# Kernel optimization log

Hardware: AMD Instinct MI355X
Metric: run time of the kernel (lower is better)

The kernel has to match this reference:

```python
import jax, jax.numpy as jnp
import numpy as np

HID = 512

def setup_inputs() -> dict:
    key = jax.random.key(0)
    k1, k2, k3, k4, k5, k6 = jax.random.split(key, 6)
    B, T, H = 32, 4096, HID
    enc_seq = jax.random.normal(k1, (B, T, H), dtype=jnp.float32)
    enc_mask = jax.random.randint(k2, (B, T), 0, 2, dtype=jnp.int32)
    dec_state = jax.random.normal(k3, (B, H), dtype=jnp.float32)
    # Linear weights, torch layout: y = x @ W.T
    scale = 1.0 / np.sqrt(H)
    W_h = jax.random.uniform(k4, (H, H), jnp.float32, -scale, scale)
    W_s = jax.random.uniform(k5, (H, H), jnp.float32, -scale, scale)
    v = jax.random.uniform(k6, (H,), jnp.float32, -scale, scale)
    return {"enc_seq": enc_seq, "enc_mask": enc_mask, "dec_state": dec_state,
            "W_h": W_h, "W_s": W_s, "v": v}

def reference(enc_seq, enc_mask, dec_state, W_h, W_s, v):
    # s: [B,H] -> [B,1,H] broadcast over T; h: [B,T,H]
    s = jnp.einsum('bh,kh->bk', dec_state, W_s)[:, None, :]
    h = jnp.einsum('bth,kh->btk', enc_seq, W_h)
    e = jnp.einsum('bth,h->bt', jnp.tanh(h + s), v)  # [B,T]
    e = jnp.where(enc_mask == 0, jnp.float32(-1e9), e)
    a = jax.nn.softmax(e, axis=1)  # [B,T]
    ctx = jnp.einsum('bt,bth->bh', a, enc_seq)  # [B,H]
    return (ctx, a)
```

## Files before the change

kernel.cpp:

```cpp
#include <hip/hip_runtime.h>
#include <hip/hip_bf16.h>
#include <cstdint>
#include <cstddef>

#define HID 512
#define T_SZ 4096

typedef __bf16 bf16x8 __attribute__((ext_vector_type(8)));
typedef float f32x4 __attribute__((ext_vector_type(4)));

__device__ __forceinline__ unsigned short f2bf_rne(float f) {
    unsigned int u = __float_as_uint(f);
    unsigned int r = (u + 0x7FFFu + ((u >> 16) & 1u)) >> 16;
    return (unsigned short)r;
}

__device__ __forceinline__ bf16x8 pack8(float4 x0, float4 x1) {
    bf16x8 r;
    r[0] = (__bf16)x0.x; r[1] = (__bf16)x0.y; r[2] = (__bf16)x0.z; r[3] = (__bf16)x0.w;
    r[4] = (__bf16)x1.x; r[5] = (__bf16)x1.y; r[6] = (__bf16)x1.z; r[7] = (__bf16)x1.w;
    return r;
}

__device__ __forceinline__ float fast_tanh(float x) {
    float e = __expf(2.0f * x);
    return 1.0f - 2.0f / (e + 1.0f);
}

__device__ __forceinline__ void gload_lds16(const void* g, void* l) {
    __builtin_amdgcn_global_load_lds(
        (const __attribute__((address_space(1))) unsigned int*)g,
        (__attribute__((address_space(3))) unsigned int*)l, 16, 0, 0);
}

__global__ void k_s(const float* __restrict__ dec, const float* __restrict__ Ws,
                    float* __restrict__ s) {
    int idx = blockIdx.x * 256 + threadIdx.x;
    int b = idx >> 9, n = idx & 511;
    const float4* dp = reinterpret_cast<const float4*>(dec + (size_t)b * HID);
    const float4* wp = reinterpret_cast<const float4*>(Ws + (size_t)n * HID);
    float acc = 0.f;
#pragma unroll 8
    for (int i = 0; i < HID / 4; ++i) {
        float4 d = dp[i], w = wp[i];
        acc += d.x * w.x + d.y * w.y + d.z * w.z + d.w * w.w;
    }
    s[idx] = acc;
}

__global__ void k_pack(const float* __restrict__ Wh, uint4* __restrict__ Wb) {
    int idx = blockIdx.x * 256 + threadIdx.x;
    int n = idx >> 6;
    int k0 = (idx & 63) * 8;
    const float4* p = reinterpret_cast<const float4*>(Wh + (size_t)n * HID + k0);
    float4 x0 = p[0], x1 = p[1];
    uint4 w;
    w.x = f2bf_rne(x0.x) | ((unsigned)f2bf_rne(x0.y) << 16);
    w.y = f2bf_rne(x0.z) | ((unsigned)f2bf_rne(x0.w) << 16);
    w.z = f2bf_rne(x1.x) | ((unsigned)f2bf_rne(x1.y) << 16);
    w.w = f2bf_rne(x1.z) | ((unsigned)f2bf_rne(x1.w) << 16);
    int n4 = n >> 4, c = n & 15, kk = k0 >> 5, g = (k0 >> 3) & 3;
    Wb[(size_t)kk * 2048 + n4 * 64 + g * 16 + c] = w;
}

__global__ void __launch_bounds__(512, 2) k_gemm_e(
    const float* __restrict__ enc, const uint4* __restrict__ Wb,
    const float* __restrict__ s, const float* __restrict__ v,
    float* __restrict__ part_e) {
    __shared__ __align__(16) unsigned char Abuf[2][32768];
    __shared__ __align__(16) unsigned char Bbuf[2][32768];
    __shared__ float red[4][256];

    const int tid = threadIdx.x;
    const int p = blockIdx.x;
    const int logical = (p & 7) * 128 + (p >> 3);
    const int h = logical & 1;
    const int mt = logical >> 1;
    const size_t row0 = (size_t)mt * 256;
    const int b = (int)(row0 >> 12);

    const int lane = tid & 63, wid = tid >> 6;
    const int c16 = lane & 15, g4 = lane >> 4;
    const int wm = wid >> 2, wn = wid & 3;

    float sv_s[4], sv_v[4];
#pragma unroll
    for (int ni = 0; ni < 4; ++ni) {
        int n = h * 256 + wn * 64 + ni * 16 + c16;
        sv_s[ni] = s[b * HID + n];
        sv_v[ni] = v[n];
    }

    const float* Asrc[4];
    int Adst[4];
#pragma unroll
    for (int i = 0; i < 4; ++i) {
        int ch = tid + i * 512;
        int kk2 = ch >> 10, rem = ch & 1023;
        int rt = rem >> 6, g = (rem >> 4) & 3, cc = rem & 15;
        Asrc[i] = enc + (row0 + rt * 16 + cc) * HID + kk2 * 32 + g * 8;
        Adst[i] = ch * 16;
    }

    float4 ar[8];

#pragma unroll
    for (int r = 0; r < 4; ++r) {
        int j = wid * 4 + r, kk2 = j >> 4, n4o = j & 15;
        gload_lds16(Wb + (size_t)kk2 * 2048 + (h * 16 + n4o) * 64 + lane,
                    &Bbuf[0][(kk2 * 1024 + n4o * 64) * 16]);
    }
#pragma unroll
    for (int i = 0; i < 4; ++i) {
        ar[2 * i]     = *reinterpret_cast<const float4*>(Asrc[i]);
        ar[2 * i + 1] = *reinterpret_cast<const float4*>(Asrc[i] + 4);
    }
#pragma unroll
    for (int i = 0; i < 4; ++i)
        *reinterpret_cast<bf16x8*>(&Abuf[0][Adst[i]]) = pack8(ar[2 * i], ar[2 * i + 1]);
    asm volatile("s_waitcnt lgkmcnt(0)\n\ts_barrier" ::: "memory");

    f32x4 acc[8][4] = {};

#pragma unroll
    for (int t = 0; t < 8; ++t) {
        const int cur = t & 1, nxt = cur ^ 1;
        if (t < 7) {
#pragma unroll
            for (int r = 0; r < 4; ++r) {
                int j = wid * 4 + r, kk2 = j >> 4, n4o = j & 15;
                gload_lds16(Wb + (size_t)(2 * (t + 1) + kk2) * 2048
                                + (h * 16 + n4o) * 64 + lane,
                            &Bbuf[nxt][(kk2 * 1024 + n4o * 64) * 16]);
            }
#pragma unroll
            for (int i = 0; i < 4; ++i) {
                ar[2 * i]     = *reinterpret_cast<const float4*>(Asrc[i] + (t + 1) * 64);
                ar[2 * i + 1] = *reinterpret_cast<const float4*>(Asrc[i] + (t + 1) * 64 + 4);
            }
        }
#pragma unroll
        for (int kk2 = 0; kk2 < 2; ++kk2) {
            bf16x8 bfr[4];
#pragma unroll
            for (int ni = 0; ni < 4; ++ni)
                bfr[ni] = *reinterpret_cast<const bf16x8*>(
                    &Bbuf[cur][(kk2 * 1024 + (wn * 4 + ni) * 64 + lane) * 16]);
#pragma unroll
            for (int mh = 0; mh < 2; ++mh) {
                bf16x8 afr[4];
#pragma unroll
                for (int i = 0; i < 4; ++i)
                    afr[i] = *reinterpret_cast<const bf16x8*>(
                        &Abuf[cur][(kk2 * 1024 + (wm * 8 + mh * 4 + i) * 64 + lane) * 16]);
                __builtin_amdgcn_s_setprio(1);
#pragma unroll
                for (int i = 0; i < 4; ++i)
#pragma unroll
                    for (int ni = 0; ni < 4; ++ni)
                        acc[mh * 4 + i][ni] = __builtin_amdgcn_mfma_f32_16x16x32_bf16(
                            afr[i], bfr[ni], acc[mh * 4 + i][ni], 0, 0, 0);
                __builtin_amdgcn_s_setprio(0);
            }
        }
        if (t < 7) {
            __builtin_amdgcn_sched_barrier(0);
#pragma unroll
            for (int i = 0; i < 4; ++i)
                *reinterpret_cast<bf16x8*>(&Abuf[nxt][Adst[i]]) =
                    pack8(ar[2 * i], ar[2 * i + 1]);
            asm volatile("s_waitcnt lgkmcnt(0)\n\ts_barrier" ::: "memory");
        }
    }

    float e_part[8][4] = {};
#pragma unroll
    for (int ni = 0; ni < 4; ++ni) {
        float sn = sv_s[ni], vn = sv_v[ni];
#pragma unroll
        for (int mi = 0; mi < 8; ++mi)
#pragma unroll
            for (int r = 0; r < 4; ++r)
                e_part[mi][r] += fast_tanh(acc[mi][ni][r] + sn) * vn;
    }
#pragma unroll
    for (int mm = 1; mm <= 8; mm <<= 1)
#pragma unroll
        for (int mi = 0; mi < 8; ++mi)
#pragma unroll
            for (int r = 0; r < 4; ++r)
                e_part[mi][r] += __shfl_xor(e_part[mi][r], mm);

    if (c16 == 0) {
#pragma unroll
        for (int mi = 0; mi < 8; ++mi)
#pragma unroll
            for (int r = 0; r < 4; ++r)
                red[wn][wm * 128 + mi * 16 + g4 * 4 + r] = e_part[mi][r];
    }
    __syncthreads();
    if (tid < 256)
        part_e[(size_t)h * 131072 + row0 + tid] =
            red[0][tid] + red[1][tid] + red[2][tid] + red[3][tid];
}

__global__ void k_softmax(const float* __restrict__ part_e, float* __restrict__ a,
                          const int* __restrict__ mask) {
    int b = blockIdx.x, tid = threadIdx.x;
    int lane = tid & 63, wid = tid >> 6;
    __shared__ float red[16];
    float vals[4]; int ms[4];
    float mx = -1e30f;
#pragma unroll
    for (int j = 0; j < 4; ++j) {
        size_t t = (size_t)b * T_SZ + tid + j * 1024;
        vals[j] = part_e[t] + part_e[131072 + t];
        ms[j] = mask[t];
        if (ms[j]) mx = fmaxf(mx, vals[j]);
    }
#pragma unroll
    for (int m = 32; m >= 1; m >>= 1) mx = fmaxf(mx, __shfl_xor(mx, m));
    if (lane == 0) red[wid] = mx;
    __syncthreads();
    if (tid == 0) {
        float m2 = red[0];
        for (int i = 1; i < 16; ++i) m2 = fmaxf(m2, red[i]);
        red[0] = m2;
    }
    __syncthreads();
    mx = red[0];
    __syncthreads();
    float pv[4]; float sum = 0.f;
#pragma unroll
    for (int j = 0; j < 4; ++j) { pv[j] = ms[j] ? __expf(vals[j] - mx) : 0.f; sum += pv[j]; }
#pragma unroll
    for (int m = 32; m >= 1; m >>= 1) sum += __shfl_xor(sum, m);
    if (lane == 0) red[wid] = sum;
    __syncthreads();
    if (tid == 0) {
        float s2 = 0.f;
        for (int i = 0; i < 16; ++i) s2 += red[i];
        red[0] = s2;
    }
    __syncthreads();
    float inv = 1.f / red[0];
#pragma unroll
    for (int j = 0; j < 4; ++j)
        a[(size_t)b * T_SZ + tid + j * 1024] = pv[j] * inv;
}

__global__ void k_ctx(const float* __restrict__ enc, const float* __restrict__ a,
                      float2* __restrict__ part) {
    int ts = blockIdx.x, b = blockIdx.y, tid = threadIdx.x;
    size_t rbase = (size_t)b * T_SZ + (size_t)ts * 128;
    const float2* ep = reinterpret_cast<const float2*>(enc + rbase * HID) + tid;
    const float* ap = a + rbase;
    float ax = 0.f, ay = 0.f, bx = 0.f, by = 0.f;
#pragma unroll 2
    for (int t = 0; t < 128; t += 2) {
        float a0 = ap[t], a1 = ap[t + 1];
        float2 e0 = ep[(size_t)t * 256], e1 = ep[(size_t)(t + 1) * 256];
        ax += a0 * e0.x; ay += a0 * e0.y;
        bx += a1 * e1.x; by += a1 * e1.y;
    }
    float2 r; r.x = ax + bx; r.y = ay + by;
    part[(size_t)(b * 32 + ts) * 256 + tid] = r;
}

__global__ void k_ctxred(const float* __restrict__ part, float* __restrict__ ctx) {
    int idx = blockIdx.x * 256 + threadIdx.x;
    int b = idx >> 9, h = idx & 511;
    float sum = 0.f;
#pragma unroll
    for (int ts = 0; ts < 32; ++ts) sum += part[(size_t)(b * 32 + ts) * 512 + h];
    ctx[idx] = sum;
}

extern "C" void kernel_launch(void* const* d_in, const int* in_sizes, int n_in,
                              void* d_out, int out_size, void* d_ws, size_t ws_size,
                              hipStream_t stream) {
    const float* enc  = (const float*)d_in[0];
    const int*   mask = (const int*)d_in[1];
    const float* dec  = (const float*)d_in[2];
    const float* Wh   = (const float*)d_in[3];
    const float* Ws   = (const float*)d_in[4];
    const float* v    = (const float*)d_in[5];

    float* out = (float*)d_out;
    float* ctx = out;
    float* a   = out + 16384;

    float* ws     = (float*)d_ws;
    float* s      = ws;
    uint4* Wb     = (uint4*)(ws + 16384);
    float* part_e = ws + 16384 + 131072;
    float* part   = part_e + 262144;

    hipLaunchKernelGGL(k_s,      dim3(64),      dim3(256),  0, stream, dec, Ws, s);
    hipLaunchKernelGGL(k_pack,   dim3(128),     dim3(256),  0, stream, Wh, Wb);
    hipLaunchKernelGGL(k_gemm_e, dim3(1024),    dim3(512),  0, stream, enc, Wb, s, v, part_e);
    hipLaunchKernelGGL(k_softmax,dim3(32),      dim3(1024), 0, stream, part_e, a, mask);
    hipLaunchKernelGGL(k_ctx,    dim3(32, 32),  dim3(256),  0, stream, enc, a, (float2*)part);
    hipLaunchKernelGGL(k_ctxred, dim3(64),      dim3(256),  0, stream, part, ctx);
}
```

Before: 217.7 us.

## Deepen A-tile prefetch to two stages and drop dedicated reduction LDS

The GEMM kernel now holds the A tile for step t+1 in registers while issuing global loads for step t+2, and packs the previous registers into LDS before the MFMA loop instead of after it. The end-of-step barrier waits with vmcnt(8) so outstanding A loads can stay in flight across steps. The reduction scratch array is aliased onto the A buffer, and launch bounds drop from 2 to 1 blocks per CU, giving more registers for the extra prefetch state at the cost of occupancy.

```diff
diff --git a/kernel.cpp b/kernel.cpp
--- a/kernel.cpp
+++ b/kernel.cpp
@@ -63,20 +63,18 @@
     Wb[(size_t)kk * 2048 + n4 * 64 + g * 16 + c] = w;
 }
 
-__global__ void __launch_bounds__(512, 2) k_gemm_e(
+__global__ void __launch_bounds__(512, 1) k_gemm_e(
     const float* __restrict__ enc, const uint4* __restrict__ Wb,
     const float* __restrict__ s, const float* __restrict__ v,
     float* __restrict__ part_e) {
     __shared__ __align__(16) unsigned char Abuf[2][32768];
     __shared__ __align__(16) unsigned char Bbuf[2][32768];
-    __shared__ float red[4][256];
 
     const int tid = threadIdx.x;
     const int p = blockIdx.x;
     const int logical = (p & 7) * 128 + (p >> 3);
     const int h = logical & 1;
-    const int mt = logical >> 1;
-    const size_t row0 = (size_t)mt * 256;
+    const size_t row0 = (size_t)(logical >> 1) * 256;
     const int b = (int)(row0 >> 12);
 
     const int lane = tid & 63, wid = tid >> 6;
@@ -95,29 +93,44 @@
     int Adst[4];
 #pragma unroll
     for (int i = 0; i < 4; ++i) {
-        int ch = tid + i * 512;
-        int kk2 = ch >> 10, rem = ch & 1023;
-        int rt = rem >> 6, g = (rem >> 4) & 3, cc = rem & 15;
-        Asrc[i] = enc + (row0 + rt * 16 + cc) * HID + kk2 * 32 + g * 8;
+        int ch = i * 512 + tid;
+        int kh = ch >> 10, cl = ch & 1023;
+        int mf = cl >> 6, g = (cl >> 4) & 3, c = cl & 15;
+        Asrc[i] = enc + (row0 + mf * 16 + c) * HID + kh * 32 + g * 8;
         Adst[i] = ch * 16;
     }
 
-    float4 ar[8];
-
+    const uint4* Bsrc[4];
+    int Bdst[4];
 #pragma unroll
     for (int r = 0; r < 4; ++r) {
-        int j = wid * 4 + r, kk2 = j >> 4, n4o = j & 15;
-        gload_lds16(Wb + (size_t)kk2 * 2048 + (h * 16 + n4o) * 64 + lane,
-                    &Bbuf[0][(kk2 * 1024 + n4o * 64) * 16]);
-    }
-#pragma unroll
-    for (int i = 0; i < 4; ++i) {
-        ar[2 * i]     = *reinterpret_cast<const float4*>(Asrc[i]);
-        ar[2 * i + 1] = *reinterpret_cast<const float4*>(Asrc[i] + 4);
-    }
-#pragma unroll
-    for (int i = 0; i < 4; ++i)
-        *reinterpret_cast<bf16x8*>(&Abuf[0][Adst[i]]) = pack8(ar[2 * i], ar[2 * i + 1]);
+        int j = r * 8 + wid, khb = j >> 4, nf = j & 15;
+        Bsrc[r] = Wb + (size_t)khb * 2048 + (h * 16 + nf) * 64 + lane;
+        Bdst[r] = (khb * 1024 + nf * 64) * 16;
+    }
+
+    float4 aR[8];
+
+#pragma unroll
+    for (int r = 0; r < 4; ++r)
+        gload_lds16(Bsrc[r], &Bbuf[0][Bdst[r]]);
+    {
+        float4 a0[8];
+#pragma unroll
+        for (int i = 0; i < 4; ++i) {
+            a0[2 * i]     = *reinterpret_cast<const float4*>(Asrc[i]);
+            a0[2 * i + 1] = *reinterpret_cast<const float4*>(Asrc[i] + 4);
+        }
+#pragma unroll
+        for (int i = 0; i < 4; ++i) {
+            aR[2 * i]     = *reinterpret_cast<const float4*>(Asrc[i] + 64);
+            aR[2 * i + 1] = *reinterpret_cast<const float4*>(Asrc[i] + 68);
+        }
+#pragma unroll
+        for (int i = 0; i < 4; ++i)
+            *reinterpret_cast<bf16x8*>(&Abuf[0][Adst[i]]) =
+                pack8(a0[2 * i], a0[2 * i + 1]);
+    }
     asm volatile("s_waitcnt lgkmcnt(0)\n\ts_barrier" ::: "memory");
 
     f32x4 acc[8][4] = {};
@@ -127,32 +140,32 @@
         const int cur = t & 1, nxt = cur ^ 1;
         if (t < 7) {
 #pragma unroll
-            for (int r = 0; r < 4; ++r) {
-                int j = wid * 4 + r, kk2 = j >> 4, n4o = j & 15;
-                gload_lds16(Wb + (size_t)(2 * (t + 1) + kk2) * 2048
-                                + (h * 16 + n4o) * 64 + lane,
-                            &Bbuf[nxt][(kk2 * 1024 + n4o * 64) * 16]);
-            }
+            for (int r = 0; r < 4; ++r)
+                gload_lds16(Bsrc[r] + (size_t)(t + 1) * 4096, &Bbuf[nxt][Bdst[r]]);
 #pragma unroll
             for (int i = 0; i < 4; ++i) {
-                ar[2 * i]     = *reinterpret_cast<const float4*>(Asrc[i] + (t + 1) * 64);
-                ar[2 * i + 1] = *reinterpret_cast<const float4*>(Asrc[i] + (t + 1) * 64 + 4);
+                *reinterpret_cast<bf16x8*>(&Abuf[nxt][Adst[i]]) =
+                    pack8(aR[2 * i], aR[2 * i + 1]);
+                if (t < 6) {
+                    aR[2 * i]     = *reinterpret_cast<const float4*>(Asrc[i] + (t + 2) * 64);
+                    aR[2 * i + 1] = *reinterpret_cast<const float4*>(Asrc[i] + (t + 2) * 64 + 4);
+                }
             }
         }
 #pragma unroll
-        for (int kk2 = 0; kk2 < 2; ++kk2) {
+        for (int kh = 0; kh < 2; ++kh) {
             bf16x8 bfr[4];
 #pragma unroll
             for (int ni = 0; ni < 4; ++ni)
                 bfr[ni] = *reinterpret_cast<const bf16x8*>(
-                    &Bbuf[cur][(kk2 * 1024 + (wn * 4 + ni) * 64 + lane) * 16]);
+                    &Bbuf[cur][(kh * 1024 + (wn * 4 + ni) * 64 + lane) * 16]);
 #pragma unroll
             for (int mh = 0; mh < 2; ++mh) {
                 bf16x8 afr[4];
 #pragma unroll
                 for (int i = 0; i < 4; ++i)
                     afr[i] = *reinterpret_cast<const bf16x8*>(
-                        &Abuf[cur][(kk2 * 1024 + (wm * 8 + mh * 4 + i) * 64 + lane) * 16]);
+                        &Abuf[cur][(kh * 1024 + (wm * 8 + mh * 4 + i) * 64 + lane) * 16]);
                 __builtin_amdgcn_s_setprio(1);
 #pragma unroll
                 for (int i = 0; i < 4; ++i)
@@ -163,14 +176,10 @@
                 __builtin_amdgcn_s_setprio(0);
             }
         }
-        if (t < 7) {
-            __builtin_amdgcn_sched_barrier(0);
-#pragma unroll
-            for (int i = 0; i < 4; ++i)
-                *reinterpret_cast<bf16x8*>(&Abuf[nxt][Adst[i]]) =
-                    pack8(ar[2 * i], ar[2 * i + 1]);
-            asm volatile("s_waitcnt lgkmcnt(0)\n\ts_barrier" ::: "memory");
-        }
+        if (t < 6)
+            asm volatile("s_waitcnt vmcnt(8) lgkmcnt(0)\n\ts_barrier" ::: "memory");
+        else if (t == 6)
+            asm volatile("s_waitcnt vmcnt(0) lgkmcnt(0)\n\ts_barrier" ::: "memory");
     }
 
     float e_part[8][4] = {};
@@ -178,30 +187,32 @@
     for (int ni = 0; ni < 4; ++ni) {
         float sn = sv_s[ni], vn = sv_v[ni];
 #pragma unroll
-        for (int mi = 0; mi < 8; ++mi)
+        for (int mf = 0; mf < 8; ++mf)
 #pragma unroll
             for (int r = 0; r < 4; ++r)
-                e_part[mi][r] += fast_tanh(acc[mi][ni][r] + sn) * vn;
+                e_part[mf][r] += fast_tanh(acc[mf][ni][r] + sn) * vn;
     }
 #pragma unroll
     for (int mm = 1; mm <= 8; mm <<= 1)
 #pragma unroll
-        for (int mi = 0; mi < 8; ++mi)
+        for (int mf = 0; mf < 8; ++mf)
 #pragma unroll
             for (int r = 0; r < 4; ++r)
-                e_part[mi][r] += __shfl_xor(e_part[mi][r], mm);
-
+                e_part[mf][r] += __shfl_xor(e_part[mf][r], mm);
+
+    __syncthreads();
+    float* red = reinterpret_cast<float*>(&Abuf[0][0]);
     if (c16 == 0) {
 #pragma unroll
-        for (int mi = 0; mi < 8; ++mi)
+        for (int mf = 0; mf < 8; ++mf)
 #pragma unroll
             for (int r = 0; r < 4; ++r)
-                red[wn][wm * 128 + mi * 16 + g4 * 4 + r] = e_part[mi][r];
+                red[wn * 256 + wm * 128 + mf * 16 + g4 * 4 + r] = e_part[mf][r];
     }
     __syncthreads();
     if (tid < 256)
         part_e[(size_t)h * 131072 + row0 + tid] =
-            red[0][tid] + red[1][tid] + red[2][tid] + red[3][tid];
+            red[tid] + red[256 + tid] + red[512 + tid] + red[768 + tid];
 }
 
 __global__ void k_softmax(const float* __restrict__ part_e, float* __restrict__ a,
```

After: 242.7 us. +11.5%, slower.
